# Optimization experiments

Hardware: AMD Instinct MI355X
Metric: run time of the kernel (lower is better)

## Reference

```python
import jax, jax.numpy as jnp
import numpy as np

N_NODES = 50000
N_EDGES = 800000
IN_DIM = 256
OUT_DIM = 32
HEADS = 4
NEG_SLOPE = 0.2  # PyG GATConv default
LN_EPS = 1e-5


def setup_inputs() -> dict:
    key = jax.random.key(0)
    ks = jax.random.split(key, 8)
    x = jax.random.normal(ks[0], (N_NODES, IN_DIM), dtype=jnp.float32)
    edge_index = jax.random.randint(ks[1], (2, N_EDGES), 0, N_NODES, dtype=jnp.int64)
    # Glorot-ish scaling for stability
    W = jax.random.normal(ks[2], (IN_DIM, HEADS * OUT_DIM), dtype=jnp.float32) / np.sqrt(IN_DIM)
    att_src = jax.random.normal(ks[3], (HEADS, OUT_DIM), dtype=jnp.float32) / np.sqrt(OUT_DIM)
    att_dst = jax.random.normal(ks[4], (HEADS, OUT_DIM), dtype=jnp.float32) / np.sqrt(OUT_DIM)
    bias = jax.random.normal(ks[5], (HEADS * OUT_DIM,), dtype=jnp.float32) * 0.02
    gamma = jnp.ones((HEADS * OUT_DIM,), dtype=jnp.float32)
    beta = jnp.zeros((HEADS * OUT_DIM,), dtype=jnp.float32)
    return {"x": x, "edge_index": edge_index, "W": W, "att_src": att_src,
            "att_dst": att_dst, "bias": bias, "gamma": gamma, "beta": beta}


def reference(x, edge_index, W, att_src, att_dst, bias, gamma, beta):
    N = x.shape[0]
    H, C = att_src.shape
    # --- GATConv (PyG semantics, eval mode so attention dropout is identity) ---
    # add self-loops (PyG default add_self_loops=True)
    loops = jnp.arange(N, dtype=edge_index.dtype)
    src = jnp.concatenate([edge_index[0], loops])  # [E+N]
    dst = jnp.concatenate([edge_index[1], loops])
    h = (x @ W).reshape(N, H, C)                    # [N,H,C] (lin has no bias)
    a_s = jnp.einsum('nhc,hc->nh', h, att_src)      # [N,H]
    a_d = jnp.einsum('nhc,hc->nh', h, att_dst)
    e = jax.nn.leaky_relu(a_s[src] + a_d[dst], NEG_SLOPE)  # [E+N,H]
    # segment softmax over incoming edges of each destination node
    emax = jax.ops.segment_max(e, dst, num_segments=N)     # every node has a self-loop
    ee = jnp.exp(e - emax[dst])
    denom = jax.ops.segment_sum(ee, dst, num_segments=N)
    alpha = ee / denom[dst]                                 # [E+N,H]
    msg = h[src] * alpha[:, :, None]                        # [E+N,H,C]
    out = jax.ops.segment_sum(msg, dst, num_segments=N).reshape(N, H * C) + bias
    # --- LayerNorm ---
    mu = out.mean(-1, keepdims=True)
    var = ((out - mu) ** 2).mean(-1, keepdims=True)
    out = (out - mu) * jax.lax.rsqrt(var + LN_EPS) * gamma + beta
    # --- dropout (eval: identity) + ELU ---
    return jax.nn.elu(out)
```

## Files before the change

kernel.cpp:

```cpp
#include <hip/hip_runtime.h>
#include <hip/hip_bf16.h>
#include <cstdint>
#include <cstddef>

#define N_NODES 50000
#define N_EDGES 800000
#define IN_DIM 256
#define HC 128
#define HEADS 4
#define NEG_SLOPE 0.2f
#define LN_EPS 1e-5f

#define NGB ((N_NODES + 63) / 64)
#define CAP 64
#define NBUCK 196
#define CAP_PB 32

typedef _Float16 f16x8 __attribute__((ext_vector_type(8)));
typedef _Float16 f16x2 __attribute__((ext_vector_type(2)));
typedef float f32x4 __attribute__((ext_vector_type(4)));

__device__ __forceinline__ float lrelu(float x) { return x > 0.f ? x : NEG_SLOPE * x; }
__device__ __forceinline__ unsigned pack_h2(float a, float b) {
    f16x2 h; h[0] = (_Float16)a; h[1] = (_Float16)b;
    return *(unsigned*)&h;
}

__global__ __launch_bounds__(256) void k_fused(
    const float* __restrict__ x, const float* __restrict__ W,
    const int* __restrict__ ei,
    const float* __restrict__ att_src, const float* __restrict__ att_dst,
    _Float16* __restrict__ h16, float* __restrict__ a_s, float* __restrict__ a_d,
    int* __restrict__ cnt_tab, int2* __restrict__ arena)
{
    __shared__ _Float16 Wlds[32768];
    const int tid = threadIdx.x;
    const int b = blockIdx.x;

    if (b & 1) {
        int* cnt = (int*)Wlds;
        const int blk = b >> 1;
        const int eb = blk << 10;
        cnt[tid] = 0;
        __syncthreads();
        int src[4], dst[4], rk[4], bk[4];
        bool valid[4];
#pragma unroll
        for (int it = 0; it < 4; ++it) {
            int e = eb + it * 256 + tid;
            valid[it] = (e < N_EDGES);
            src[it] = 0; dst[it] = 0; bk[it] = 0; rk[it] = 0;
            if (valid[it]) {
                src[it] = ei[e];
                dst[it] = ei[N_EDGES + e];
                bk[it]  = dst[it] >> 8;
                rk[it]  = atomicAdd(&cnt[bk[it]], 1);
            }
        }
#pragma unroll
        for (int it = 0; it < 4; ++it) {
            if (valid[it]) {
                int p = ((bk[it] * NGB + blk) << 5) + rk[it];
                arena[p] = (int2){src[it], dst[it]};
            }
        }
        __syncthreads();
        if (tid < NBUCK) cnt_tab[blk * NBUCK + tid] = cnt[tid];
        return;
    }

    const int gb   = b >> 1;
    const int wave = tid >> 6;
    const int lane = tid & 63;
    const int col  = lane & 15;
    const int quad = lane >> 4;
    const int m0   = gb * 64 + wave * 16;

    const int rowA = min(m0 + col, N_NODES - 1);
    const float* xrow = x + (size_t)rowA * IN_DIM + quad * 8;

    float4 xr[16];
#pragma unroll
    for (int kt = 0; kt < 8; ++kt) {
        xr[2 * kt]     = *(const float4*)(xrow + kt * 32);
        xr[2 * kt + 1] = *(const float4*)(xrow + kt * 32 + 4);
    }

    {
#pragma unroll
        for (int it = 0; it < 16; ++it) {
            int c = it * 256 + tid;
            int ccol = c & 15, cquad = (c >> 4) & 3, cnt_ = (c >> 6) & 7, ckt = c >> 9;
            const float* wp = W + (size_t)(ckt * 32 + cquad * 8) * HC + cnt_ * 16 + ccol;
            f16x8 v;
#pragma unroll
            for (int j = 0; j < 8; ++j) v[j] = (_Float16)wp[j * HC];
            *(f16x8*)(Wlds + (size_t)c * 8) = v;
        }
    }
    __syncthreads();

    f32x4 acc[8];
#pragma unroll
    for (int nt = 0; nt < 8; ++nt) acc[nt] = (f32x4){0.f, 0.f, 0.f, 0.f};

#pragma unroll
    for (int kt = 0; kt < 8; ++kt) {
        float4 xa = xr[2 * kt], xb = xr[2 * kt + 1];
        f16x8 a;
        a[0] = (_Float16)xa.x; a[1] = (_Float16)xa.y;
        a[2] = (_Float16)xa.z; a[3] = (_Float16)xa.w;
        a[4] = (_Float16)xb.x; a[5] = (_Float16)xb.y;
        a[6] = (_Float16)xb.z; a[7] = (_Float16)xb.w;
#pragma unroll
        for (int nt = 0; nt < 8; ++nt) {
            f16x8 bb = *(const f16x8*)&Wlds[((kt * 8 + nt) * 64 + quad * 16 + col) * 8];
            acc[nt] = __builtin_amdgcn_mfma_f32_16x16x32_f16(a, bb, acc[nt], 0, 0, 0);
        }
    }

    f16x2* h2g = (f16x2*)h16;
#pragma unroll
    for (int a2 = 0; a2 < 4; ++a2) {
#pragma unroll
        for (int r = 0; r < 4; ++r) {
            int row = m0 + quad * 4 + r;
            if (row < N_NODES) {
                f16x2 hv;
                hv[0] = (_Float16)acc[2 * a2][r];
                hv[1] = (_Float16)acc[2 * a2 + 1][r];
                h2g[(size_t)row * 64 + a2 * 16 + col] = hv;
            }
        }
    }

    float pS[4][4], pD[4][4];
#pragma unroll
    for (int hd = 0; hd < 4; ++hd)
#pragma unroll
        for (int r = 0; r < 4; ++r) { pS[hd][r] = 0.f; pD[hd][r] = 0.f; }

#pragma unroll
    for (int nt = 0; nt < 8; ++nt) {
        int ch = nt * 16 + col;
        float sv = att_src[ch], dv = att_dst[ch];
        int hd = nt >> 1;
#pragma unroll
        for (int r = 0; r < 4; ++r) {
            pS[hd][r] += acc[nt][r] * sv;
            pD[hd][r] += acc[nt][r] * dv;
        }
    }
#pragma unroll
    for (int off = 1; off < 16; off <<= 1) {
#pragma unroll
        for (int hd = 0; hd < 4; ++hd)
#pragma unroll
            for (int r = 0; r < 4; ++r) {
                pS[hd][r] += __shfl_xor(pS[hd][r], off, 16);
                pD[hd][r] += __shfl_xor(pD[hd][r], off, 16);
            }
    }
    if (col == 0) {
#pragma unroll
        for (int r = 0; r < 4; ++r) {
            int row = m0 + quad * 4 + r;
            if (row < N_NODES) {
#pragma unroll
                for (int hd = 0; hd < 4; ++hd) {
                    a_s[row * HEADS + hd] = pS[hd][r];
                    a_d[row * HEADS + hd] = pD[hd][r];
                }
            }
        }
    }
}

__global__ __launch_bounds__(1024) void k_bucket(
    const int2* __restrict__ arena, const int* __restrict__ cnt_tab,
    int* __restrict__ rec, int* __restrict__ counts)
{
    __shared__ int cnt[256];
    const int b = blockIdx.x, tid = threadIdx.x;
    if (tid < 256) cnt[tid] = 0;
    __syncthreads();
    if (tid < NGB) {
        int m = cnt_tab[tid * NBUCK + b];
        const int2* seg = arena + (((size_t)b * NGB + tid) << 5);
        for (int i = 0; i < m; ++i) {
            int2 ed = seg[i];
            int r = atomicAdd(&cnt[ed.y & 255], 1);
            rec[((size_t)ed.y << 6) + r] = ed.x;
        }
    }
    __syncthreads();
    if (tid < 256) {
        int n = (b << 8) + tid;
        if (n < N_NODES) counts[n] = cnt[tid];
    }
}

__global__ __launch_bounds__(256) void k_gather(
    const int* __restrict__ counts, const int* __restrict__ rec,
    const float* __restrict__ a_s, const float* __restrict__ a_d,
    const _Float16* __restrict__ h16, const float* __restrict__ bias,
    const float* __restrict__ gamma, const float* __restrict__ beta,
    float* __restrict__ out)
{
    __shared__ int   lsrc[256];
    __shared__ uint2 lw[256];

    int gid = blockIdx.x * 256 + threadIdx.x;
    int n = gid >> 6, lane = gid & 63;
    if (n >= N_NODES) return;

    const int wbase = (threadIdx.x >> 6) * 64;
    const int beg = n << 6;
    const int deg = counts[n];
    const int hd = lane >> 4;
    const f16x2* h2 = (const f16x2*)h16;
    const unsigned short* lwh = (const unsigned short*)&lw[wbase];

    const float4 ad4 = *(const float4*)(a_d + (size_t)n * HEADS);
    const float adh = (hd == 0) ? ad4.x : (hd == 1) ? ad4.y : (hd == 2) ? ad4.z : ad4.w;
    const float wSelf = __expf(lrelu(a_s[n * HEADS + hd] + adh));
    float den = wSelf;
    f16x2 hv = h2[(size_t)n * 64 + lane];
    float acc0 = (float)hv[0] * wSelf;
    float acc1 = (float)hv[1] * wSelf;

    for (int base = 0; base < deg; base += 64) {
        int nc = min(64, deg - base);
        if (lane < nc) {
            int src = rec[beg + base + lane];
            lsrc[wbase + lane] = src;
            float4 s4 = *(const float4*)(a_s + (size_t)src * HEADS);
            float w0 = __expf(lrelu(s4.x + ad4.x));
            float w1 = __expf(lrelu(s4.y + ad4.y));
            float w2 = __expf(lrelu(s4.z + ad4.z));
            float w3 = __expf(lrelu(s4.w + ad4.w));
            lw[wbase + lane] = (uint2){pack_h2(w0, w1), pack_h2(w2, w3)};
        }
        int j = 0;
        for (; j + 8 <= nc; j += 8) {
            int s[8]; float w[8]; f16x2 hh[8];
#pragma unroll
            for (int k = 0; k < 8; ++k) {
                s[k] = lsrc[wbase + j + k];
                unsigned short uw = lwh[(j + k) * 4 + hd];
                _Float16 wf = *(_Float16*)&uw;
                w[k] = (float)wf;
            }
#pragma unroll
            for (int k = 0; k < 8; ++k) hh[k] = h2[(size_t)s[k] * 64 + lane];
#pragma unroll
            for (int k = 0; k < 8; ++k) {
                acc0 += (float)hh[k][0] * w[k];
                acc1 += (float)hh[k][1] * w[k];
                den  += w[k];
            }
        }
        for (; j < nc; ++j) {
            int s0 = lsrc[wbase + j];
            unsigned short uw = lwh[j * 4 + hd];
            _Float16 wf = *(_Float16*)&uw;
            float w0 = (float)wf;
            f16x2 hx = h2[(size_t)s0 * 64 + lane];
            acc0 += (float)hx[0] * w0;
            acc1 += (float)hx[1] * w0;
            den  += w0;
        }
    }

    const int c0 = (lane >> 4) * 32 + (lane & 15);
    const int c1 = c0 + 16;
    float v0 = acc0 / den + bias[c0];
    float v1 = acc1 / den + bias[c1];
    float s = v0 + v1;
#pragma unroll
    for (int off = 32; off; off >>= 1) s += __shfl_xor(s, off, 64);
    float mu = s * (1.f / 128.f);
    float d0 = v0 - mu, d1 = v1 - mu;
    float q = d0 * d0 + d1 * d1;
#pragma unroll
    for (int off = 32; off; off >>= 1) q += __shfl_xor(q, off, 64);
    float rs = rsqrtf(q * (1.f / 128.f) + LN_EPS);
    float o0 = d0 * rs * gamma[c0] + beta[c0];
    float o1 = d1 * rs * gamma[c1] + beta[c1];
    o0 = o0 > 0.f ? o0 : __expf(o0) - 1.f;
    o1 = o1 > 0.f ? o1 : __expf(o1) - 1.f;
    out[(size_t)n * HC + c0] = o0;
    out[(size_t)n * HC + c1] = o1;
}

extern "C" void kernel_launch(void* const* d_in, const int* in_sizes, int n_in,
                              void* d_out, int out_size, void* d_ws, size_t ws_size,
                              hipStream_t stream) {
    const float* x       = (const float*)d_in[0];
    const int*   ei      = (const int*)d_in[1];
    const float* W       = (const float*)d_in[2];
    const float* att_src = (const float*)d_in[3];
    const float* att_dst = (const float*)d_in[4];
    const float* bias    = (const float*)d_in[5];
    const float* gamma   = (const float*)d_in[6];
    const float* beta    = (const float*)d_in[7];
    float* out = (float*)d_out;

    char* ws = (char*)d_ws;
    _Float16* h16     = (_Float16*)(ws);
    float*    a_s     = (float*)(ws + 12800000);
    float*    a_d     = (float*)(ws + 13600000);
    int*      rec     = (int*)  (ws + 14400000);
    int*      counts  = (int*)  (ws + 27200000);
    int*      cnt_tab = (int*)  (ws + 27400000);
    int2*     arena   = (int2*) (ws + 28020000);

    k_fused<<<2 * NGB, 256, 0, stream>>>(x, W, ei, att_src, att_dst,
                                         h16, a_s, a_d, cnt_tab, arena);
    k_bucket<<<NBUCK, 1024, 0, stream>>>(arena, cnt_tab, rec, counts);
    k_gather<<<(N_NODES * 64 + 255) / 256, 256, 0, stream>>>(
        counts, rec, a_s, a_d, h16, bias, gamma, beta, out);
}
```

Before: 186.9 us.

## Pre-convert W to fp16 once and split edge binning from GEMM kernel

The fused kernel, which interleaved GEMM blocks with edge-binning blocks, is split in two. A new prep kernel converts W to fp16 in the MFMA-friendly layout once, and also does the edge bucketing pass. The GEMM kernel then copies the pre-swizzled W16 into LDS with wide vector loads, instead of every block doing strided fp32 loads and conversions. This removes per-block redundant conversion but adds one kernel launch, and the GEMM and binning work no longer overlap within one launch.

```diff
diff --git a/kernel.cpp b/kernel.cpp
--- a/kernel.cpp
+++ b/kernel.cpp
@@ -26,55 +26,71 @@
     return *(unsigned*)&h;
 }
 
-__global__ __launch_bounds__(256) void k_fused(
-    const float* __restrict__ x, const float* __restrict__ W,
-    const int* __restrict__ ei,
+__global__ __launch_bounds__(256) void k_prep_passA(
+    const float* __restrict__ W, const int* __restrict__ ei,
+    _Float16* __restrict__ W16,
+    int* __restrict__ cnt_tab, int2* __restrict__ arena)
+{
+    __shared__ int cnt[256];
+    const int tid = threadIdx.x;
+    const int b = blockIdx.x;
+
+    if (b < 16) {
+        int c = b * 256 + tid;
+        int col = c & 15, quad = (c >> 4) & 3, nt = (c >> 6) & 7, kt = c >> 9;
+        int n = nt * 16 + col;
+        f16x8 v;
+#pragma unroll
+        for (int j = 0; j < 8; ++j) {
+            int k = kt * 32 + quad * 8 + j;
+            v[j] = (_Float16)W[k * HC + n];
+        }
+        *(f16x8*)(W16 + (size_t)c * 8) = v;
+        return;
+    }
+
+    const int blk = b - 16;
+    const int eb = blk << 10;
+    cnt[tid] = 0;
+    __syncthreads();
+    int src[4], dst[4], rk[4], bk[4];
+    bool valid[4];
+#pragma unroll
+    for (int it = 0; it < 4; ++it) {
+        int e = eb + it * 256 + tid;
+        valid[it] = (e < N_EDGES);
+        src[it] = 0; dst[it] = 0; bk[it] = 0; rk[it] = 0;
+        if (valid[it]) {
+            src[it] = ei[e];
+            dst[it] = ei[N_EDGES + e];
+            bk[it]  = dst[it] >> 8;
+            rk[it]  = atomicAdd(&cnt[bk[it]], 1);
+        }
+    }
+#pragma unroll
+    for (int it = 0; it < 4; ++it) {
+        if (valid[it]) {
+            int p = ((bk[it] * NGB + blk) << 5) + rk[it];
+            arena[p] = (int2){src[it], dst[it]};
+        }
+    }
+    __syncthreads();
+    if (tid < NBUCK) cnt_tab[blk * NBUCK + tid] = cnt[tid];
+}
+
+__global__ __launch_bounds__(256) void k_gemm(
+    const float* __restrict__ x, const _Float16* __restrict__ W16,
     const float* __restrict__ att_src, const float* __restrict__ att_dst,
-    _Float16* __restrict__ h16, float* __restrict__ a_s, float* __restrict__ a_d,
-    int* __restrict__ cnt_tab, int2* __restrict__ arena)
+    _Float16* __restrict__ h16, float* __restrict__ a_s, float* __restrict__ a_d)
 {
     __shared__ _Float16 Wlds[32768];
     const int tid = threadIdx.x;
-    const int b = blockIdx.x;
-
-    if (b & 1) {
-        int* cnt = (int*)Wlds;
-        const int blk = b >> 1;
-        const int eb = blk << 10;
-        cnt[tid] = 0;
-        __syncthreads();
-        int src[4], dst[4], rk[4], bk[4];
-        bool valid[4];
-#pragma unroll
-        for (int it = 0; it < 4; ++it) {
-            int e = eb + it * 256 + tid;
-            valid[it] = (e < N_EDGES);
-            src[it] = 0; dst[it] = 0; bk[it] = 0; rk[it] = 0;
-            if (valid[it]) {
-                src[it] = ei[e];
-                dst[it] = ei[N_EDGES + e];
-                bk[it]  = dst[it] >> 8;
-                rk[it]  = atomicAdd(&cnt[bk[it]], 1);
-            }
-        }
-#pragma unroll
-        for (int it = 0; it < 4; ++it) {
-            if (valid[it]) {
-                int p = ((bk[it] * NGB + blk) << 5) + rk[it];
-                arena[p] = (int2){src[it], dst[it]};
-            }
-        }
-        __syncthreads();
-        if (tid < NBUCK) cnt_tab[blk * NBUCK + tid] = cnt[tid];
-        return;
-    }
-
-    const int gb   = b >> 1;
+
     const int wave = tid >> 6;
     const int lane = tid & 63;
     const int col  = lane & 15;
     const int quad = lane >> 4;
-    const int m0   = gb * 64 + wave * 16;
+    const int m0   = blockIdx.x * 64 + wave * 16;
 
     const int rowA = min(m0 + col, N_NODES - 1);
     const float* xrow = x + (size_t)rowA * IN_DIM + quad * 8;
@@ -87,16 +103,10 @@
     }
 
     {
-#pragma unroll
-        for (int it = 0; it < 16; ++it) {
-            int c = it * 256 + tid;
-            int ccol = c & 15, cquad = (c >> 4) & 3, cnt_ = (c >> 6) & 7, ckt = c >> 9;
-            const float* wp = W + (size_t)(ckt * 32 + cquad * 8) * HC + cnt_ * 16 + ccol;
-            f16x8 v;
-#pragma unroll
-            for (int j = 0; j < 8; ++j) v[j] = (_Float16)wp[j * HC];
-            *(f16x8*)(Wlds + (size_t)c * 8) = v;
-        }
+        const uint4* g4 = (const uint4*)W16;
+        uint4* s4 = (uint4*)Wlds;
+#pragma unroll
+        for (int it = 0; it < 16; ++it) s4[it * 256 + tid] = g4[it * 256 + tid];
     }
     __syncthreads();
 
@@ -314,9 +324,10 @@
     int*      counts  = (int*)  (ws + 27200000);
     int*      cnt_tab = (int*)  (ws + 27400000);
     int2*     arena   = (int2*) (ws + 28020000);
-
-    k_fused<<<2 * NGB, 256, 0, stream>>>(x, W, ei, att_src, att_dst,
-                                         h16, a_s, a_d, cnt_tab, arena);
+    _Float16* W16     = (_Float16*)(ws + 67260000);
+
+    k_prep_passA<<<16 + NGB, 256, 0, stream>>>(W, ei, W16, cnt_tab, arena);
+    k_gemm<<<NGB, 256, 0, stream>>>(x, W16, att_src, att_dst, h16, a_s, a_d);
     k_bucket<<<NBUCK, 1024, 0, stream>>>(arena, cnt_tab, rec, counts);
     k_gather<<<(N_NODES * 64 + 255) / 256, 256, 0, stream>>>(
         counts, rec, a_s, a_d, h16, bias, gamma, beta, out);
```

Result: faster. 177.2 us (-5.2%).
